# Kernel tuning notes

Hardware: AMD Instinct MI355X
Metric: run time of the kernel (lower is better)

## Reference

```python
import jax, jax.numpy as jnp
import numpy as np

B, S, D, H, O = 64, 512, 1024, 1024, 1024


def setup_inputs() -> dict:
    key = jax.random.key(0)
    ks = jax.random.split(key, 7)
    s_in = 1.0 / np.sqrt(D)
    s_h = 1.0 / np.sqrt(H)
    return {
        "x": jax.random.normal(ks[0], (B, S, D), dtype=jnp.float32),
        # gate order along axis 0: i, f, o, c_candidate
        "Wx": jax.random.uniform(ks[1], (4, H, D), jnp.float32, -s_in, s_in),
        "bx": jax.random.uniform(ks[2], (4, H), jnp.float32, -s_in, s_in),
        "Wh": jax.random.uniform(ks[3], (4, H, H), jnp.float32, -s_h, s_h),
        "bh": jax.random.uniform(ks[4], (4, H), jnp.float32, -s_h, s_h),
        "Wp": jax.random.uniform(ks[5], (O, H), jnp.float32, -s_h, s_h),
        "bp": jax.random.uniform(ks[6], (O,), jnp.float32, -s_h, s_h),
    }


def reference(x, Wx, bx, Wh, bh, Wp, bp):
    b, s, d = x.shape
    h_dim = Wh.shape[-1]
    # Precompute all input-to-hidden gate projections in one big GEMM:
    # equivalent to W_i(x_t)+b, W_f(x_t)+b, W_o(x_t)+b, W_c(x_t)+b per step.
    xg = jnp.einsum('bsd,ghd->sbgh', x, Wx) + bx  # [S, B, 4, H]

    def step(carry, xg_t):
        c, h = carry
        # hidden-to-hidden projections for all 4 gates, fused
        g = xg_t + jnp.einsum('bh,gkh->bgk', h, Wh) + bh  # [B, 4, H]
        i = jax.nn.sigmoid(g[:, 0])
        f = jax.nn.sigmoid(g[:, 1])
        o = jax.nn.sigmoid(g[:, 2])
        c_cand = jnp.tanh(g[:, 3])
        c_new = f * c + i * c_cand
        h_new = o * jnp.tanh(c_new)
        y = h_new @ Wp.T + bp  # [B, O]
        return (c_new, h_new), y

    init = (jnp.zeros((b, h_dim), x.dtype), jnp.zeros((b, h_dim), x.dtype))
    (c, h), ys = jax.lax.scan(step, init, xg)
    outputs = jnp.transpose(ys, (1, 0, 2))  # [B, S, O]
    return outputs, (c, h)
```

## Files before the change

kernel.cpp:

```cpp
#include <hip/hip_runtime.h>


typedef unsigned short u16;
typedef u16   u16x4  __attribute__((ext_vector_type(4)));
typedef u16   u16x8  __attribute__((ext_vector_type(8)));
typedef __bf16 bf16x8 __attribute__((ext_vector_type(8)));
typedef float f32x4  __attribute__((ext_vector_type(4)));

__device__ __forceinline__ u16 f2bf(float x) {
    unsigned u = __float_as_uint(x);
    u = (u + 0x7FFFu + ((u >> 16) & 1u)) >> 16;
    return (u16)u;
}
__device__ __forceinline__ float bf2f(u16 h) {
    return __uint_as_float(((unsigned)h) << 16);
}
__device__ __forceinline__ float fsig(float x) { return 1.f / (1.f + __expf(-x)); }
__device__ __forceinline__ float ftanh(float x) { return 1.f - 2.f / (__expf(2.f * x) + 1.f); }


__global__ void k_convert_x(const float* __restrict__ x, u16* __restrict__ xb) {
    int bi = blockIdx.x;
    int b = bi >> 9, s = bi & 511;
    const float4* src = (const float4*)(x + (size_t)bi * 1024);
    u16* dst = xb + ((size_t)(s * 64 + b)) * 1024;
    int t = threadIdx.x;
    float4 v = src[t];
    u16x4 o; o.x = f2bf(v.x); o.y = f2bf(v.y); o.z = f2bf(v.z); o.w = f2bf(v.w);
    *(u16x4*)(dst + t * 4) = o;
}

__global__ void k_pack_gates(const float* __restrict__ w, u16* __restrict__ wp) {
    int np = blockIdx.x;
    int g = np & 3, k = np >> 2;
    const float4* src = (const float4*)(w + ((size_t)(g * 1024 + k)) * 1024);
    u16* dst = wp + (size_t)np * 1024;
    int t = threadIdx.x;
    float4 v = src[t];
    u16x4 o; o.x = f2bf(v.x); o.y = f2bf(v.y); o.z = f2bf(v.z); o.w = f2bf(v.w);
    *(u16x4*)(dst + t * 4) = o;
}

__global__ void k_f2bf(const float* __restrict__ src, u16* __restrict__ dst, int n) {
    int i = (blockIdx.x * 256 + threadIdx.x) * 4;
    if (i < n) {
        float4 v = *(const float4*)(src + i);
        u16x4 o; o.x = f2bf(v.x); o.y = f2bf(v.y); o.z = f2bf(v.z); o.w = f2bf(v.w);
        *(u16x4*)(dst + i) = o;
    }
}

__global__ void k_bias(const float* __restrict__ bx, const float* __restrict__ bh,
                       float* __restrict__ bias) {
    int np = blockIdx.x * 256 + threadIdx.x;
    int g = np & 3, k = np >> 2;
    bias[np] = bx[g * 1024 + k] + bh[g * 1024 + k];
}

__global__ void k_init(u16* __restrict__ hall0, float* __restrict__ cstate) {
    int i = blockIdx.x * 256 + threadIdx.x;
    hall0[i] = 0;
    cstate[i] = 0.f;
}

__global__ __launch_bounds__(256) void k_gemm64(
    const u16* __restrict__ A, const u16* __restrict__ Bt,
    int K, int N, int mode,
    u16* __restrict__ Cb,
    float* __restrict__ Cf, const float* __restrict__ bp, int S_, int O_) {
    __shared__ u16 As[64 * 72];
    __shared__ u16 Bs[64 * 72];
    int mb = blockIdx.x, nb = blockIdx.y;
    int tid = threadIdx.x, w = tid >> 6, lane = tid & 63;
    f32x4 acc[4] = {};
    int kchunks = K >> 6;
    for (int kc = 0; kc < kchunks; ++kc) {
        int k0 = kc * 64;
#pragma unroll
        for (int r = 0; r < 2; ++r) {
            int c = tid + 256 * r;
            int row = c >> 3, kk = (c & 7) * 8;
            *(u16x8*)(&As[row * 72 + kk]) =
                *(const u16x8*)(A + (size_t)(mb * 64 + row) * K + k0 + kk);
            *(u16x8*)(&Bs[row * 72 + kk]) =
                *(const u16x8*)(Bt + (size_t)(nb * 64 + row) * K + k0 + kk);
        }
        __syncthreads();
#pragma unroll
        for (int kk = 0; kk < 64; kk += 32) {
            bf16x8 a = *(const bf16x8*)(&As[(w * 16 + (lane & 15)) * 72 + kk + (lane >> 4) * 8]);
#pragma unroll
            for (int nt = 0; nt < 4; ++nt) {
                bf16x8 b = *(const bf16x8*)(&Bs[(nt * 16 + (lane & 15)) * 72 + kk + (lane >> 4) * 8]);
                acc[nt] = __builtin_amdgcn_mfma_f32_16x16x32_bf16(a, b, acc[nt], 0, 0, 0);
            }
        }
        __syncthreads();
    }
    int q = lane >> 4, cl = lane & 15;
    if (mode == 0) {
#pragma unroll
        for (int nt = 0; nt < 4; ++nt)
#pragma unroll
            for (int j = 0; j < 4; ++j) {
                int m = mb * 64 + w * 16 + q * 4 + j;
                int n = nb * 64 + nt * 16 + cl;
                Cb[(size_t)m * N + n] = f2bf(acc[nt][j]);
            }
    } else {
#pragma unroll
        for (int nt = 0; nt < 4; ++nt)
#pragma unroll
            for (int j = 0; j < 4; ++j) {
                int m = mb * 64 + w * 16 + q * 4 + j;
                int n = nb * 64 + nt * 16 + cl;
                int b = m & 63, s = m >> 6;
                Cf[((size_t)b * S_ + s) * O_ + n] = acc[nt][j] + bp[n];
            }
    }
}

__global__ __launch_bounds__(256) void k_step(
    const u16* __restrict__ hprev,
    const u16* __restrict__ whp,
    const u16* __restrict__ xgt,
    const float* __restrict__ bias,
    float* __restrict__ cstate,
    float* __restrict__ hf32,
    u16* __restrict__ hnext) {
    __shared__ u16 As[64 * 264];
    __shared__ u16 Bs[16 * 264];
    __shared__ float glds[64 * 20];
    int nb = blockIdx.x;
    int tid = threadIdx.x, w = tid >> 6, lane = tid & 63;
    f32x4 acc = {};
    for (int kc = 0; kc < 4; ++kc) {
        int k0 = kc * 256;
#pragma unroll
        for (int r = 0; r < 8; ++r) {
            int c = tid + 256 * r;
            int row = c >> 5, kk = (c & 31) * 8;
            *(u16x8*)(&As[row * 264 + kk]) =
                *(const u16x8*)(hprev + (size_t)row * 1024 + k0 + kk);
        }
#pragma unroll
        for (int r = 0; r < 2; ++r) {
            int c = tid + 256 * r;
            int row = c >> 5, kk = (c & 31) * 8;
            *(u16x8*)(&Bs[row * 264 + kk]) =
                *(const u16x8*)(whp + (size_t)(nb * 16 + row) * 1024 + k0 + kk);
        }
        __syncthreads();
#pragma unroll
        for (int kk = 0; kk < 256; kk += 32) {
            bf16x8 a = *(const bf16x8*)(&As[(w * 16 + (lane & 15)) * 264 + kk + (lane >> 4) * 8]);
            bf16x8 b = *(const bf16x8*)(&Bs[(lane & 15) * 264 + kk + (lane >> 4) * 8]);
            acc = __builtin_amdgcn_mfma_f32_16x16x32_bf16(a, b, acc, 0, 0, 0);
        }
        __syncthreads();
    }
    int q = lane >> 4, cl = lane & 15;
#pragma unroll
    for (int j = 0; j < 4; ++j) {
        int row = w * 16 + q * 4 + j;
        int n = nb * 16 + cl;
        glds[row * 20 + cl] = acc[j] + bf2f(xgt[(size_t)row * 4096 + n]) + bias[n];
    }
    __syncthreads();
    {
        int row = tid >> 2, kv = tid & 3;
        float4 gv = *(const float4*)(&glds[row * 20 + kv * 4]);
        float ig = fsig(gv.x), fg = fsig(gv.y), og = fsig(gv.z), cc = ftanh(gv.w);
        int k = nb * 4 + kv;
        float c_old = cstate[row * 1024 + k];
        float c_new = fg * c_old + ig * cc;
        cstate[row * 1024 + k] = c_new;
        float h = og * ftanh(c_new);
        hf32[row * 1024 + k] = h;
        hnext[row * 1024 + k] = f2bf(h);
    }
}

__global__ void k_tail(const float* __restrict__ cstate, const float* __restrict__ hf32,
                       float* __restrict__ out) {
    int i = blockIdx.x * 256 + threadIdx.x;
    if (i < 65536) out[33554432 + i] = cstate[i];
    else           out[33554432 + i] = hf32[i - 65536];
}

extern "C" void kernel_launch(void* const* d_in, const int* in_sizes, int n_in,
                              void* d_out, int out_size, void* d_ws, size_t ws_size,
                              hipStream_t stream) {
    const float* x  = (const float*)d_in[0];
    const float* Wx = (const float*)d_in[1];
    const float* bx = (const float*)d_in[2];
    const float* Wh = (const float*)d_in[3];
    const float* bh = (const float*)d_in[4];
    const float* Wp = (const float*)d_in[5];
    const float* bp = (const float*)d_in[6];
    float* out = (float*)d_out;
    char* ws = (char*)d_ws;

    u16*   xb   = (u16*)  (ws);
    u16*   wxp  = (u16*)  (ws + 67108864);
    u16*   whp  = (u16*)  (ws + 75497472);
    u16*   wpb  = (u16*)  (ws + 83886080);
    float* bias = (float*)(ws + 85983232);
    float* cst  = (float*)(ws + 85999616);
    float* hf32 = (float*)(ws + 86261760);
    u16*   xg   = (u16*)  (ws + 86523904);
    u16*   hall = (u16*)  (ws + 354959360);

    k_convert_x<<<32768, 256, 0, stream>>>(x, xb);
    k_pack_gates<<<4096, 256, 0, stream>>>(Wx, wxp);
    k_pack_gates<<<4096, 256, 0, stream>>>(Wh, whp);
    k_f2bf<<<1024, 256, 0, stream>>>(Wp, wpb, 1048576);
    k_bias<<<16, 256, 0, stream>>>(bx, bh, bias);
    k_init<<<256, 256, 0, stream>>>(hall, cst);

    k_gemm64<<<dim3(512, 64), 256, 0, stream>>>(xb, wxp, 1024, 4096, 0,
                                                xg, nullptr, nullptr, 0, 0);
    for (int t = 0; t < 512; ++t) {
        k_step<<<256, 256, 0, stream>>>(hall + (size_t)t * 65536, whp,
                                        xg + (size_t)t * 64 * 4096, bias,
                                        cst, hf32, hall + (size_t)(t + 1) * 65536);
    }
    k_gemm64<<<dim3(512, 16), 256, 0, stream>>>(hall + 65536, wpb, 1024, 1024, 1,
                                                nullptr, out, bp, 512, 1024);
    k_tail<<<512, 256, 0, stream>>>(cst, hf32, out);
}
```

Baseline: 4.998 ms.

## Replace per-timestep launches with persistent kernel using grid barrier

Replaces 512 separate step-kernel launches with one persistent kernel of 256 blocks that loops over timesteps and synchronizes through a two-level atomic grid barrier kept in scratch space at the start of the output buffer. Each block keeps its slice of the recurrent weights resident in LDS for all steps, reads the hidden state directly from global memory into MFMA operands, and holds the cell state in registers. This removes the per-step launch overhead and the repeated weight reloads. In exchange it relies on all 256 blocks being co-resident, and on barrier counters in the output buffer that are later overwritten by the projection GEMM.

Result: slower. 12.30 ms (+146.0%).

```diff
diff --git a/kernel.cpp b/kernel.cpp
--- a/kernel.cpp
+++ b/kernel.cpp
@@ -51,8 +51,9 @@
 }
 
 __global__ void k_bias(const float* __restrict__ bx, const float* __restrict__ bh,
-                       float* __restrict__ bias) {
+                       float* __restrict__ bias, unsigned* __restrict__ bar) {
     int np = blockIdx.x * 256 + threadIdx.x;
+    if (np < 34) bar[np] = 0u;
     int g = np & 3, k = np >> 2;
     bias[np] = bx[g * 1024 + k] + bh[g * 1024 + k];
 }
@@ -120,64 +121,91 @@
     }
 }
 
-__global__ __launch_bounds__(256) void k_step(
-    const u16* __restrict__ hprev,
+__global__ __launch_bounds__(256) void k_steps(
     const u16* __restrict__ whp,
-    const u16* __restrict__ xgt,
+    const u16* __restrict__ xg,
     const float* __restrict__ bias,
     float* __restrict__ cstate,
     float* __restrict__ hf32,
-    u16* __restrict__ hnext) {
-    __shared__ u16 As[64 * 264];
-    __shared__ u16 Bs[16 * 264];
+    u16* __restrict__ hall,
+    unsigned* __restrict__ bar) {
+    __shared__ u16 Bs[16 * 1032];
     __shared__ float glds[64 * 20];
     int nb = blockIdx.x;
     int tid = threadIdx.x, w = tid >> 6, lane = tid & 63;
-    f32x4 acc = {};
-    for (int kc = 0; kc < 4; ++kc) {
-        int k0 = kc * 256;
-#pragma unroll
-        for (int r = 0; r < 8; ++r) {
-            int c = tid + 256 * r;
-            int row = c >> 5, kk = (c & 31) * 8;
-            *(u16x8*)(&As[row * 264 + kk]) =
-                *(const u16x8*)(hprev + (size_t)row * 1024 + k0 + kk);
-        }
-#pragma unroll
-        for (int r = 0; r < 2; ++r) {
-            int c = tid + 256 * r;
-            int row = c >> 5, kk = (c & 31) * 8;
-            *(u16x8*)(&Bs[row * 264 + kk]) =
-                *(const u16x8*)(whp + (size_t)(nb * 16 + row) * 1024 + k0 + kk);
-        }
+    int q = lane >> 4, cl = lane & 15;
+
+#pragma unroll
+    for (int r = 0; r < 8; ++r) {
+        int c = tid + 256 * r;
+        int row = c >> 7, kk = (c & 127) * 8;
+        *(u16x8*)(&Bs[row * 1032 + kk]) =
+            *(const u16x8*)(whp + (size_t)(nb * 16 + row) * 1024 + kk);
+    }
+    float biasv = bias[nb * 16 + cl];
+    int erow = tid >> 2, ekv = tid & 3, ek = nb * 4 + ekv;
+    float creg = 0.f;
+    int boff = cl * 1032 + q * 8;
+    __syncthreads();
+
+    for (int t = 0; t < 512; ++t) {
+        const u16* hp  = hall + (size_t)t * 65536;
+        const u16* xgt = xg + (size_t)t * 262144;
+        float xv[4];
+#pragma unroll
+        for (int j = 0; j < 4; ++j)
+            xv[j] = bf2f(xgt[(size_t)(w * 16 + q * 4 + j) * 4096 + nb * 16 + cl]);
+
+        const u16* arow = hp + (size_t)(w * 16 + cl) * 1024 + q * 8;
+        f32x4 acc0 = {}, acc1 = {};
+#pragma unroll
+        for (int kk = 0; kk < 1024; kk += 64) {
+            bf16x8 a0 = *(const bf16x8*)(arow + kk);
+            bf16x8 b0 = *(const bf16x8*)(&Bs[boff + kk]);
+            acc0 = __builtin_amdgcn_mfma_f32_16x16x32_bf16(a0, b0, acc0, 0, 0, 0);
+            bf16x8 a1 = *(const bf16x8*)(arow + kk + 32);
+            bf16x8 b1 = *(const bf16x8*)(&Bs[boff + kk + 32]);
+            acc1 = __builtin_amdgcn_mfma_f32_16x16x32_bf16(a1, b1, acc1, 0, 0, 0);
+        }
+#pragma unroll
+        for (int j = 0; j < 4; ++j)
+            glds[(w * 16 + q * 4 + j) * 20 + cl] = acc0[j] + acc1[j] + xv[j] + biasv;
         __syncthreads();
-#pragma unroll
-        for (int kk = 0; kk < 256; kk += 32) {
-            bf16x8 a = *(const bf16x8*)(&As[(w * 16 + (lane & 15)) * 264 + kk + (lane >> 4) * 8]);
-            bf16x8 b = *(const bf16x8*)(&Bs[(lane & 15) * 264 + kk + (lane >> 4) * 8]);
-            acc = __builtin_amdgcn_mfma_f32_16x16x32_bf16(a, b, acc, 0, 0, 0);
-        }
-        __syncthreads();
-    }
-    int q = lane >> 4, cl = lane & 15;
-#pragma unroll
-    for (int j = 0; j < 4; ++j) {
-        int row = w * 16 + q * 4 + j;
-        int n = nb * 16 + cl;
-        glds[row * 20 + cl] = acc[j] + bf2f(xgt[(size_t)row * 4096 + n]) + bias[n];
-    }
-    __syncthreads();
-    {
-        int row = tid >> 2, kv = tid & 3;
-        float4 gv = *(const float4*)(&glds[row * 20 + kv * 4]);
-        float ig = fsig(gv.x), fg = fsig(gv.y), og = fsig(gv.z), cc = ftanh(gv.w);
-        int k = nb * 4 + kv;
-        float c_old = cstate[row * 1024 + k];
-        float c_new = fg * c_old + ig * cc;
-        cstate[row * 1024 + k] = c_new;
-        float h = og * ftanh(c_new);
-        hf32[row * 1024 + k] = h;
-        hnext[row * 1024 + k] = f2bf(h);
+
+        {
+            float4 gv = *(const float4*)(&glds[erow * 20 + ekv * 4]);
+            float ig = fsig(gv.x), fg = fsig(gv.y), og = fsig(gv.z), cc = ftanh(gv.w);
+            float c_new = fg * creg + ig * cc;
+            creg = c_new;
+            float h = og * ftanh(c_new);
+            hall[(size_t)(t + 1) * 65536 + erow * 1024 + ek] = f2bf(h);
+            if (t == 511) {
+                cstate[erow * 1024 + ek] = c_new;
+                hf32[erow * 1024 + ek]   = h;
+            }
+        }
+
+        if (t < 511) {
+            __syncthreads();
+            if (tid == 0) {
+                __builtin_amdgcn_fence(__ATOMIC_RELEASE, "agent");
+                unsigned o1 = __hip_atomic_fetch_add(&bar[nb >> 3], 1u,
+                        __ATOMIC_RELAXED, __HIP_MEMORY_SCOPE_AGENT);
+                if (o1 == (unsigned)(8 * (t + 1) - 1)) {
+                    unsigned o2 = __hip_atomic_fetch_add(&bar[32], 1u,
+                            __ATOMIC_RELAXED, __HIP_MEMORY_SCOPE_AGENT);
+                    if (o2 == (unsigned)(32 * (t + 1) - 1))
+                        __hip_atomic_store(&bar[33], (unsigned)(t + 1),
+                                __ATOMIC_RELAXED, __HIP_MEMORY_SCOPE_AGENT);
+                }
+                while (__hip_atomic_load(&bar[33], __ATOMIC_RELAXED,
+                                         __HIP_MEMORY_SCOPE_AGENT)
+                       < (unsigned)(t + 1))
+                    __builtin_amdgcn_s_sleep(1);
+            }
+            __syncthreads();
+            __builtin_amdgcn_fence(__ATOMIC_ACQUIRE, "agent");
+        }
     }
 }
 
@@ -210,21 +238,18 @@
     float* hf32 = (float*)(ws + 86261760);
     u16*   xg   = (u16*)  (ws + 86523904);
     u16*   hall = (u16*)  (ws + 354959360);
+    unsigned* bar = (unsigned*)d_out;
 
     k_convert_x<<<32768, 256, 0, stream>>>(x, xb);
     k_pack_gates<<<4096, 256, 0, stream>>>(Wx, wxp);
     k_pack_gates<<<4096, 256, 0, stream>>>(Wh, whp);
     k_f2bf<<<1024, 256, 0, stream>>>(Wp, wpb, 1048576);
-    k_bias<<<16, 256, 0, stream>>>(bx, bh, bias);
+    k_bias<<<16, 256, 0, stream>>>(bx, bh, bias, bar);
     k_init<<<256, 256, 0, stream>>>(hall, cst);
 
     k_gemm64<<<dim3(512, 64), 256, 0, stream>>>(xb, wxp, 1024, 4096, 0,
                                                 xg, nullptr, nullptr, 0, 0);
-    for (int t = 0; t < 512; ++t) {
-        k_step<<<256, 256, 0, stream>>>(hall + (size_t)t * 65536, whp,
-                                        xg + (size_t)t * 64 * 4096, bias,
-                                        cst, hf32, hall + (size_t)(t + 1) * 65536);
-    }
+    k_steps<<<256, 256, 0, stream>>>(whp, xg, bias, cst, hf32, hall, bar);
     k_gemm64<<<dim3(512, 16), 256, 0, stream>>>(hall + 65536, wpb, 1024, 1024, 1,
                                                 nullptr, out, bp, 512, 1024);
     k_tail<<<512, 256, 0, stream>>>(cst, hf32, out);
```
